# Kernel optimization log

Hardware: AMD Instinct MI355X
Metric: run time of the kernel (lower is better)

Reference implementation:

```python
import jax, jax.numpy as jnp
import numpy as np

Z_DIM = 256
N_MOD = 8
CAT = Z_DIM * N_MOD          # 2048
YS = 1024
B = 4096
EPS = 1e-5


def _layer_norm(x, g, b):
    mu = jnp.mean(x, axis=-1, keepdims=True)
    var = jnp.mean((x - mu) ** 2, axis=-1, keepdims=True)
    return (x - mu) * jax.lax.rsqrt(var + EPS) * g + b


def setup_inputs() -> dict:
    key = jax.random.key(0)
    ks = jax.random.split(key, 16)
    s_cat = 1.0 / np.sqrt(CAT)
    s_ys = 1.0 / np.sqrt(YS)
    return {
        "z_stack": jax.random.normal(ks[0], (N_MOD, B, Z_DIM), jnp.float32),
        "Wq": jax.random.normal(ks[1], (CAT, CAT), jnp.float32) * s_cat,
        "bq": jnp.zeros((CAT,), jnp.float32),
        "Wk": jax.random.normal(ks[2], (CAT, CAT), jnp.float32) * s_cat,
        "bk": jnp.zeros((CAT,), jnp.float32),
        "Wv": jax.random.normal(ks[3], (CAT, CAT), jnp.float32) * s_cat,
        "bv": jnp.zeros((CAT,), jnp.float32),
        "W1": jax.random.normal(ks[4], (CAT, YS), jnp.float32) * s_cat,
        "b1": jnp.zeros((YS,), jnp.float32),
        "W2": jax.random.normal(ks[5], (YS, CAT), jnp.float32) * s_ys,
        "b2": jnp.zeros((CAT,), jnp.float32),
        "ln1_g": jnp.ones((CAT,), jnp.float32),
        "ln1_b": jnp.zeros((CAT,), jnp.float32),
        "ln2_g": jnp.ones((CAT,), jnp.float32),
        "ln2_b": jnp.zeros((CAT,), jnp.float32),
        "Wys": jax.random.normal(ks[6], (CAT, YS), jnp.float32) * s_cat,
        "bys": jnp.zeros((YS,), jnp.float32),
        "Ws": jax.random.normal(ks[7], (N_MOD, YS, Z_DIM), jnp.float32) * s_ys,
        "bs": jnp.zeros((N_MOD, Z_DIM), jnp.float32),
    }


def reference(z_stack, Wq, bq, Wk, bk, Wv, bv, W1, b1, W2, b2,
              ln1_g, ln1_b, ln2_g, ln2_b, Wys, bys, Ws, bs):
    M, Bn, Zd = z_stack.shape
    # torch.cat(z, dim=1): [B, M*Zd]
    x = jnp.transpose(z_stack, (1, 0, 2)).reshape(Bn, M * Zd)
    # self-attention over the batch dim (unscaled, as in source)
    q = x @ Wq + bq
    k = x @ Wk + bk
    v = x @ Wv + bv
    attended = jax.nn.softmax(q @ k.T, axis=-1) @ v  # [B, B] scores
    # dropout is identity in eval mode
    x = _layer_norm(x + attended, ln1_g, ln1_b)
    h = jax.nn.gelu(x @ W1 + b1, approximate=False) @ W2 + b2
    h = _layer_norm(x + h, ln2_g, ln2_b)
    yb = h @ Wys + bys                               # [B, YS]
    # per-module scaling layers, stacked output [M, B, Zd]
    y = jnp.einsum('bs,msz->mbz', yb, Ws) + bs[:, None, :]
    return y
```

## Files before the change

kernel.cpp:

```cpp
#include <hip/hip_runtime.h>
#include <hip/hip_bf16.h>
#include <cstdint>
#include <cstddef>
#include <math.h>

typedef __bf16 bf16x8 __attribute__((ext_vector_type(8)));
typedef float  f32x4  __attribute__((ext_vector_type(4)));

#define DEVI __device__ __forceinline__

static constexpr int BB = 4096;
static constexpr int CD = 2048;
static constexpr int ZD = 256;

DEVI unsigned short f2bf(float f) {
  __bf16 h = (__bf16)f;
  return __builtin_bit_cast(unsigned short, h);
}
DEVI float bf2f(unsigned short u) {
  return (float)__builtin_bit_cast(__bf16, u);
}

DEVI void gload_lds16(const void* g, void* l) {
  __builtin_amdgcn_global_load_lds(
      (__attribute__((address_space(1))) void*)(g),
      (__attribute__((address_space(3))) void*)(l), 16, 0, 0);
}

__global__ __launch_bounds__(256) void pack_x(
    const float* __restrict__ z, float* __restrict__ x,
    unsigned short* __restrict__ xh, unsigned short* __restrict__ xl) {
  const int i = (blockIdx.x * 256 + threadIdx.x) * 4;
  const int m  = i >> 20;
  const int r  = i & 1048575;
  const int b  = r >> 8;
  const int zd = r & 255;
  const float4 v = *(const float4*)(z + i);
  const size_t o = (size_t)b * CD + m * ZD + zd;
  *(float4*)(x + o) = v;
  ushort4 h, l;
  h.x = f2bf(v.x); l.x = f2bf(v.x - bf2f(h.x));
  h.y = f2bf(v.y); l.y = f2bf(v.y - bf2f(h.y));
  h.z = f2bf(v.z); l.z = f2bf(v.z - bf2f(h.z));
  h.w = f2bf(v.w); l.w = f2bf(v.w - bf2f(h.w));
  *(ushort4*)(xh + o) = h;
  *(ushort4*)(xl + o) = l;
}

template<bool LO>
__global__ void transpose_split(const float* __restrict__ in,
                                unsigned short* __restrict__ oh,
                                unsigned short* __restrict__ ol,
                                int R, int C) {
  __shared__ float tile[32][33];
  const int c0 = blockIdx.x * 32, r0 = blockIdx.y * 32;
  const int tx = threadIdx.x, ty = threadIdx.y;
#pragma unroll
  for (int k = 0; k < 4; ++k)
    tile[ty + 8 * k][tx] = in[(size_t)(r0 + ty + 8 * k) * C + (c0 + tx)];
  __syncthreads();
#pragma unroll
  for (int k = 0; k < 4; ++k) {
    const float f = tile[tx][ty + 8 * k];
    const size_t o = (size_t)(c0 + ty + 8 * k) * R + (r0 + tx);
    const unsigned short h = f2bf(f);
    oh[o] = h;
    if constexpr (LO) ol[o] = f2bf(f - bf2f(h));
  }
}

__global__ void transpose_bf16(const unsigned short* __restrict__ in,
                               unsigned short* __restrict__ outp, int R, int C) {
  __shared__ unsigned short tile[32][33];
  const int c0 = blockIdx.x * 32, r0 = blockIdx.y * 32;
  const int tx = threadIdx.x, ty = threadIdx.y;
#pragma unroll
  for (int k = 0; k < 4; ++k)
    tile[ty + 8 * k][tx] = in[(size_t)(r0 + ty + 8 * k) * C + (c0 + tx)];
  __syncthreads();
#pragma unroll
  for (int k = 0; k < 4; ++k)
    outp[(size_t)(c0 + ty + 8 * k) * R + (r0 + tx)] = tile[tx][ty + 8 * k];
}

template<int EP, bool SPLIT>
__global__ __launch_bounds__(256) void gemm_bt(
    const unsigned short* __restrict__ Ah, const unsigned short* __restrict__ Al,
    const unsigned short* __restrict__ Bh, const unsigned short* __restrict__ Bl,
    const float* __restrict__ bias,
    float* __restrict__ Cf, unsigned short* __restrict__ Cb,
    unsigned short* __restrict__ Cb2,
    int M, int N, int K) {
  constexpr int NT = SPLIT ? 4 : 2;
  __shared__ unsigned short lds[NT][128 * 32];
  const int t = threadIdx.x;
  const int lane = t & 63;
  const int w = t >> 6;
  const int wr = (w >> 1) * 64, wc = (w & 1) * 64;
  const int lr = lane & 15, kg = lane >> 4;
  const size_t Ar0 = (size_t)blockIdx.y * 128;
  const size_t Br0 = (size_t)blockIdx.x * 128;

  f32x4 acc[4][4] = {};

  for (int k0 = 0; k0 < K; k0 += 32) {
#pragma unroll
    for (int rnd = 0; rnd < 2; ++rnd) {
      const int e = t * 8 + rnd * 2048;
      const int row = e >> 5, col = e & 31;
      const size_t ga = (Ar0 + row) * (size_t)K + (k0 + col);
      const size_t gb = (Br0 + row) * (size_t)K + (k0 + col);
      const int lo = (w << 9) + rnd * 2048;
      gload_lds16(Ah + ga, &lds[0][lo]);
      gload_lds16(Bh + gb, &lds[1][lo]);
      if constexpr (SPLIT) {
        gload_lds16(Al + ga, &lds[2][lo]);
        gload_lds16(Bl + gb, &lds[3][lo]);
      }
    }
    __syncthreads();
    bf16x8 ah[4], bh[4], al[4], bl[4];
#pragma unroll
    for (int i = 0; i < 4; ++i) {
      ah[i] = *(const bf16x8*)&lds[0][((wr + i * 16 + lr) << 5) + (kg << 3)];
      bh[i] = *(const bf16x8*)&lds[1][((wc + i * 16 + lr) << 5) + (kg << 3)];
      if constexpr (SPLIT) {
        al[i] = *(const bf16x8*)&lds[2][((wr + i * 16 + lr) << 5) + (kg << 3)];
        bl[i] = *(const bf16x8*)&lds[3][((wc + i * 16 + lr) << 5) + (kg << 3)];
      }
    }
#pragma unroll
    for (int i = 0; i < 4; ++i)
#pragma unroll
      for (int j = 0; j < 4; ++j) {
        acc[i][j] = __builtin_amdgcn_mfma_f32_16x16x32_bf16(ah[i], bh[j], acc[i][j], 0, 0, 0);
        if constexpr (SPLIT) {
          acc[i][j] = __builtin_amdgcn_mfma_f32_16x16x32_bf16(ah[i], bl[j], acc[i][j], 0, 0, 0);
          acc[i][j] = __builtin_amdgcn_mfma_f32_16x16x32_bf16(al[i], bh[j], acc[i][j], 0, 0, 0);
        }
      }
    __syncthreads();
  }

  const int rb = (int)Ar0 + wr + (lane >> 4) * 4;
  const int cb = (int)Br0 + wc + lr;
#pragma unroll
  for (int i = 0; i < 4; ++i) {
#pragma unroll
    for (int j = 0; j < 4; ++j) {
      const int col = cb + j * 16;
      const float bsv = bias ? bias[col] : 0.0f;
#pragma unroll
      for (int q = 0; q < 4; ++q) {
        const int row = rb + i * 16 + q;
        const float val = acc[i][j][q] + bsv;
        const size_t o = (size_t)row * N + col;
        if constexpr (EP == 0) {
          Cf[o] = val;
        } else if constexpr (EP == 1) {
          Cb[o] = f2bf(val);
        } else if constexpr (EP == 2) {
          const float ge = 0.5f * val * (1.0f + erff(val * 0.70710678118654752f));
          Cb[o] = f2bf(ge);
        } else if constexpr (EP == 3) {
          const unsigned short h = f2bf(val);
          Cb[o] = h;
          Cb2[o] = f2bf(val - bf2f(h));
        } else {
          const size_t oo = (size_t)(col >> 8) * ((size_t)BB * ZD)
                          + (size_t)row * ZD + (col & 255);
          Cf[oo] = val;
        }
      }
    }
  }
}

__global__ __launch_bounds__(256) void softmax_rows(const float* __restrict__ S,
                                                    unsigned short* __restrict__ P) {
  const int row = blockIdx.x;
  const int t = threadIdx.x;
  const int lane = t & 63, w = t >> 6;
  const float* s = S + (size_t)row * 4096;
  float4 v[4];
  float mx = -3.4e38f;
#pragma unroll
  for (int i = 0; i < 4; ++i) {
    v[i] = *(const float4*)(s + (size_t)(t + 256 * i) * 4);
    mx = fmaxf(mx, fmaxf(fmaxf(v[i].x, v[i].y), fmaxf(v[i].z, v[i].w)));
  }
#pragma unroll
  for (int off = 32; off >= 1; off >>= 1) mx = fmaxf(mx, __shfl_xor(mx, off));
  __shared__ float redm[4], redsum[4];
  if (lane == 0) redm[w] = mx;
  __syncthreads();
  mx = fmaxf(fmaxf(redm[0], redm[1]), fmaxf(redm[2], redm[3]));
  float sum = 0.f;
#pragma unroll
  for (int i = 0; i < 4; ++i) {
    v[i].x = expf(v[i].x - mx);
    v[i].y = expf(v[i].y - mx);
    v[i].z = expf(v[i].z - mx);
    v[i].w = expf(v[i].w - mx);
    sum += v[i].x + v[i].y + v[i].z + v[i].w;
  }
#pragma unroll
  for (int off = 32; off >= 1; off >>= 1) sum += __shfl_xor(sum, off);
  if (lane == 0) redsum[w] = sum;
  __syncthreads();
  sum = redsum[0] + redsum[1] + redsum[2] + redsum[3];
  const float inv = 1.0f / sum;
  unsigned short* p = P + (size_t)row * 4096;
#pragma unroll
  for (int i = 0; i < 4; ++i) {
    ushort4 u;
    u.x = f2bf(v[i].x * inv);
    u.y = f2bf(v[i].y * inv);
    u.z = f2bf(v[i].z * inv);
    u.w = f2bf(v[i].w * inv);
    *(ushort4*)(p + (size_t)(t + 256 * i) * 4) = u;
  }
}

template<bool WF32>
__global__ __launch_bounds__(256) void ln_fused(
    const float* __restrict__ a, const float* __restrict__ b,
    const float* __restrict__ g, const float* __restrict__ be,
    float* __restrict__ of, unsigned short* __restrict__ ob) {
  const int row = blockIdx.x;
  const int t = threadIdx.x;
  const int lane = t & 63, w = t >> 6;
  const float* ar = a + (size_t)row * 2048;
  const float* br = b + (size_t)row * 2048;
  float4 x[2];
  float s = 0.f, ss = 0.f;
#pragma unroll
  for (int i = 0; i < 2; ++i) {
    const int o = (t + 256 * i) * 4;
    const float4 av = *(const float4*)(ar + o);
    const float4 bv = *(const float4*)(br + o);
    x[i].x = av.x + bv.x; x[i].y = av.y + bv.y;
    x[i].z = av.z + bv.z; x[i].w = av.w + bv.w;
    s  += x[i].x + x[i].y + x[i].z + x[i].w;
    ss += x[i].x * x[i].x + x[i].y * x[i].y + x[i].z * x[i].z + x[i].w * x[i].w;
  }
#pragma unroll
  for (int off = 32; off >= 1; off >>= 1) {
    s  += __shfl_xor(s, off);
    ss += __shfl_xor(ss, off);
  }
  __shared__ float rs[4], rss[4];
  if (lane == 0) { rs[w] = s; rss[w] = ss; }
  __syncthreads();
  s  = rs[0] + rs[1] + rs[2] + rs[3];
  ss = rss[0] + rss[1] + rss[2] + rss[3];
  const float mu  = s * (1.0f / 2048.0f);
  const float var = ss * (1.0f / 2048.0f) - mu * mu;
  const float inv = rsqrtf(var + 1e-5f);
#pragma unroll
  for (int i = 0; i < 2; ++i) {
    const int o = (t + 256 * i) * 4;
    const float4 gv  = *(const float4*)(g + o);
    const float4 bev = *(const float4*)(be + o);
    float4 y;
    y.x = (x[i].x - mu) * inv * gv.x + bev.x;
    y.y = (x[i].y - mu) * inv * gv.y + bev.y;
    y.z = (x[i].z - mu) * inv * gv.z + bev.z;
    y.w = (x[i].w - mu) * inv * gv.w + bev.w;
    if constexpr (WF32) *(float4*)(of + (size_t)row * 2048 + o) = y;
    ushort4 u;
    u.x = f2bf(y.x); u.y = f2bf(y.y); u.z = f2bf(y.z); u.w = f2bf(y.w);
    *(ushort4*)(ob + (size_t)row * 2048 + o) = u;
  }
}

extern "C" void kernel_launch(void* const* d_in, const int* in_sizes, int n_in,
                              void* d_out, int out_size, void* d_ws, size_t ws_size,
                              hipStream_t stream) {
  (void)in_sizes; (void)n_in; (void)out_size;
  const float* z    = (const float*)d_in[0];
  const float* Wq   = (const float*)d_in[1];
  const float* bq   = (const float*)d_in[2];
  const float* Wk   = (const float*)d_in[3];
  const float* bk   = (const float*)d_in[4];
  const float* Wv   = (const float*)d_in[5];
  const float* bv   = (const float*)d_in[6];
  const float* W1   = (const float*)d_in[7];
  const float* b1   = (const float*)d_in[8];
  const float* W2   = (const float*)d_in[9];
  const float* b2   = (const float*)d_in[10];
  const float* ln1g = (const float*)d_in[11];
  const float* ln1b = (const float*)d_in[12];
  const float* ln2g = (const float*)d_in[13];
  const float* ln2b = (const float*)d_in[14];
  const float* Wys  = (const float*)d_in[15];
  const float* bys  = (const float*)d_in[16];
  const float* Ws   = (const float*)d_in[17];
  const float* bs   = (const float*)d_in[18];
  float* out = (float*)d_out;
  char* ws = (char*)d_ws;

  const size_t off_x    = 0;
  const size_t off_x2bf = 0;
  const size_t off_ybbf = 16777216;
  const size_t R2       = 33554432;
  const size_t off_xhi  = R2;
  const size_t off_xlo  = R2 + 16777216;
  const size_t off_wqh  = R2 + 33554432;
  const size_t off_wql  = off_wqh + 8388608;
  const size_t off_wkh  = off_wql + 8388608;
  const size_t off_wkl  = off_wkh + 8388608;
  const size_t off_wv   = off_wkl + 8388608;
  const size_t off_S    = R2;
  const size_t off_x1f  = R2;
  const size_t off_x1bf = R2 + 33554432;
  const size_t R3       = 109051904;
  const size_t off_w1t  = R3;
  const size_t off_w2t  = R3 + 4194304;
  const size_t off_wyst = R3 + 8388608;
  const size_t off_wst  = R3 + 12582912;
  const size_t R4       = 125829120;
  const size_t off_qh   = R4;
  const size_t off_ql   = R4 + 16777216;
  const size_t off_kh   = R4 + 33554432;
  const size_t off_kl   = R4 + 50331648;
  const size_t off_P    = R4;
  const size_t off_att  = R4 + 33554432;
  const size_t off_h2   = R4;
  const size_t R5       = 192937984;
  const size_t off_vbf  = R5;
  const size_t off_vt   = R5 + 16777216;
  const size_t off_hmid = R5;
  if (ws_size < 226492416u) return;

#define F32P(o) ((float*)(ws + (o)))
#define BFP(o)  ((unsigned short*)(ws + (o)))

  const dim3 tb(32, 8);

  pack_x<<<8192, 256, 0, stream>>>(z, F32P(off_x), BFP(off_xhi), BFP(off_xlo));
  transpose_split<true ><<<dim3(64, 64), tb, 0, stream>>>(Wq, BFP(off_wqh), BFP(off_wql), 2048, 2048);
  transpose_split<true ><<<dim3(64, 64), tb, 0, stream>>>(Wk, BFP(off_wkh), BFP(off_wkl), 2048, 2048);
  transpose_split<false><<<dim3(64, 64), tb, 0, stream>>>(Wv, BFP(off_wv), nullptr, 2048, 2048);
  transpose_split<false><<<dim3(32, 64), tb, 0, stream>>>(W1, BFP(off_w1t), nullptr, 2048, 1024);
  transpose_split<false><<<dim3(64, 32), tb, 0, stream>>>(W2, BFP(off_w2t), nullptr, 1024, 2048);
  transpose_split<false><<<dim3(32, 64), tb, 0, stream>>>(Wys, BFP(off_wyst), nullptr, 2048, 1024);
  for (int m = 0; m < 8; ++m)
    transpose_split<false><<<dim3(8, 32), tb, 0, stream>>>(
        Ws + (size_t)m * 262144, BFP(off_wst) + (size_t)m * 262144, nullptr, 1024, 256);

  gemm_bt<3, true ><<<dim3(16, 32), 256, 0, stream>>>(BFP(off_xhi), BFP(off_xlo),
      BFP(off_wqh), BFP(off_wql), bq, nullptr, BFP(off_qh), BFP(off_ql), 4096, 2048, 2048);
  gemm_bt<3, true ><<<dim3(16, 32), 256, 0, stream>>>(BFP(off_xhi), BFP(off_xlo),
      BFP(off_wkh), BFP(off_wkl), bk, nullptr, BFP(off_kh), BFP(off_kl), 4096, 2048, 2048);
  gemm_bt<1, false><<<dim3(16, 32), 256, 0, stream>>>(BFP(off_xhi), nullptr,
      BFP(off_wv), nullptr, bv, nullptr, BFP(off_vbf), nullptr, 4096, 2048, 2048);
  transpose_bf16<<<dim3(64, 128), tb, 0, stream>>>(BFP(off_vbf), BFP(off_vt), 4096, 2048);

  gemm_bt<0, true ><<<dim3(32, 32), 256, 0, stream>>>(BFP(off_qh), BFP(off_ql),
      BFP(off_kh), BFP(off_kl), nullptr, F32P(off_S), nullptr, nullptr, 4096, 4096, 2048);
  softmax_rows<<<4096, 256, 0, stream>>>(F32P(off_S), BFP(off_P));
  gemm_bt<0, false><<<dim3(16, 32), 256, 0, stream>>>(BFP(off_P), nullptr,
      BFP(off_vt), nullptr, nullptr, F32P(off_att), nullptr, nullptr, 4096, 2048, 4096);
  ln_fused<true ><<<4096, 256, 0, stream>>>(F32P(off_x), F32P(off_att), ln1g, ln1b,
      F32P(off_x1f), BFP(off_x1bf));

  gemm_bt<2, false><<<dim3(8, 32), 256, 0, stream>>>(BFP(off_x1bf), nullptr,
      BFP(off_w1t), nullptr, b1, nullptr, BFP(off_hmid), nullptr, 4096, 1024, 2048);
  gemm_bt<0, false><<<dim3(16, 32), 256, 0, stream>>>(BFP(off_hmid), nullptr,
      BFP(off_w2t), nullptr, b2, F32P(off_h2), nullptr, nullptr, 4096, 2048, 1024);
  ln_fused<false><<<4096, 256, 0, stream>>>(F32P(off_x1f), F32P(off_h2), ln2g, ln2b,
      nullptr, BFP(off_x2bf));

  gemm_bt<1, false><<<dim3(8, 32), 256, 0, stream>>>(BFP(off_x2bf), nullptr,
      BFP(off_wyst), nullptr, bys, nullptr, BFP(off_ybbf), nullptr, 4096, 1024, 2048);
  gemm_bt<4, false><<<dim3(16, 32), 256, 0, stream>>>(BFP(off_ybbf), nullptr,
      BFP(off_wst), nullptr, bs, out, nullptr, nullptr, 4096, 2048, 1024);
}
```

Before: 887.9 us.

## Fuse Q/K projections into one split-bf16 GEMM with 256x256 pipelined kernel

Packs hi/lo bf16 halves of x and of the Q/K weights side by side along K, so the three-term split-precision product becomes one plain bf16 GEMM over an extended K. A new 256x256-tile, 512-thread kernel with double-buffered direct-to-LDS loads, XOR swizzle, phased barriers and setprio computes Q and K together, then the QK^T scores. The goal is to drop the separate SPLIT GEMM launches, raise MFMA utilisation and cut repeated operand loads. In exchange it needs 128KB of dynamic LDS, uses a hard-coded K schedule and grid remap, and the workspace layout is reorganised.

```diff
diff --git a/kernel.cpp b/kernel.cpp
--- a/kernel.cpp
+++ b/kernel.cpp
@@ -29,29 +29,29 @@
 
 __global__ __launch_bounds__(256) void pack_x(
     const float* __restrict__ z, float* __restrict__ x,
-    unsigned short* __restrict__ xh, unsigned short* __restrict__ xl) {
+    unsigned short* __restrict__ x2) {
   const int i = (blockIdx.x * 256 + threadIdx.x) * 4;
   const int m  = i >> 20;
   const int r  = i & 1048575;
   const int b  = r >> 8;
   const int zd = r & 255;
   const float4 v = *(const float4*)(z + i);
-  const size_t o = (size_t)b * CD + m * ZD + zd;
-  *(float4*)(x + o) = v;
+  const size_t o32 = (size_t)b * CD + m * ZD + zd;
+  *(float4*)(x + o32) = v;
   ushort4 h, l;
   h.x = f2bf(v.x); l.x = f2bf(v.x - bf2f(h.x));
   h.y = f2bf(v.y); l.y = f2bf(v.y - bf2f(h.y));
   h.z = f2bf(v.z); l.z = f2bf(v.z - bf2f(h.z));
   h.w = f2bf(v.w); l.w = f2bf(v.w - bf2f(h.w));
-  *(ushort4*)(xh + o) = h;
-  *(ushort4*)(xl + o) = l;
+  const size_t o2 = (size_t)b * 4096 + m * ZD + zd;
+  *(ushort4*)(x2 + o2) = h;
+  *(ushort4*)(x2 + o2 + 2048) = l;
 }
 
 template<bool LO>
 __global__ void transpose_split(const float* __restrict__ in,
                                 unsigned short* __restrict__ oh,
-                                unsigned short* __restrict__ ol,
-                                int R, int C) {
+                                int R, int C, int ldo) {
   __shared__ float tile[32][33];
   const int c0 = blockIdx.x * 32, r0 = blockIdx.y * 32;
   const int tx = threadIdx.x, ty = threadIdx.y;
@@ -62,10 +62,10 @@
 #pragma unroll
   for (int k = 0; k < 4; ++k) {
     const float f = tile[tx][ty + 8 * k];
-    const size_t o = (size_t)(c0 + ty + 8 * k) * R + (r0 + tx);
+    const size_t o = (size_t)(c0 + ty + 8 * k) * ldo + (r0 + tx);
     const unsigned short h = f2bf(f);
     oh[o] = h;
-    if constexpr (LO) ol[o] = f2bf(f - bf2f(h));
+    if constexpr (LO) oh[o + R] = f2bf(f - bf2f(h));
   }
 }
 
@@ -83,16 +83,196 @@
     outp[(size_t)(c0 + ty + 8 * k) * R + (r0 + tx)] = tile[tx][ty + 8 * k];
 }
 
-template<int EP, bool SPLIT>
+#define DOMFMA(QI, QJ, AF, BF)                                            \
+  {                                                                       \
+    _Pragma("unroll") for (int ks = 0; ks < 2; ++ks) {                    \
+      _Pragma("unroll") for (int f = 0; f < 4; ++f) {                     \
+        _Pragma("unroll") for (int g = 0; g < 2; ++g) {                   \
+          acc[(QI) * 4 + f][(QJ) * 2 + g] =                               \
+              __builtin_amdgcn_mfma_f32_16x16x32_bf16(                    \
+                  AF[f][ks], BF[g][ks], acc[(QI) * 4 + f][(QJ) * 2 + g],  \
+                  0, 0, 0);                                               \
+        }                                                                 \
+      }                                                                   \
+    }                                                                     \
+  }
+
+#define PH_SYNC()                                         \
+  do {                                                    \
+    __builtin_amdgcn_s_barrier();                         \
+    asm volatile("s_waitcnt lgkmcnt(0)" ::: "memory");    \
+    __builtin_amdgcn_sched_barrier(0);                    \
+    __builtin_amdgcn_s_setprio(1);                        \
+  } while (0)
+
+#define PH_END()                                          \
+  do {                                                    \
+    __builtin_amdgcn_s_setprio(0);                        \
+    __builtin_amdgcn_sched_barrier(0);                    \
+    __builtin_amdgcn_s_barrier();                         \
+  } while (0)
+
+template<int EP>
+__global__ __launch_bounds__(512, 2) void gemm256(
+    const unsigned short* __restrict__ A,
+    const unsigned short* __restrict__ Bt,
+    const float* __restrict__ bq, const float* __restrict__ bk,
+    float* __restrict__ Cf,
+    unsigned short* __restrict__ Oa, unsigned short* __restrict__ Ob) {
+  extern __shared__ char lds[];
+  constexpr int NK = 96;
+  const int t = threadIdx.x;
+  const int lane = t & 63;
+  const int w = t >> 6;
+  const int wm = w >> 2, wn = w & 3;
+  const int lr = lane & 15, kg = lane >> 4;
+  const int bid = (blockIdx.x & 7) * 32 + (blockIdx.x >> 3);
+  const int bx = bid & 15, by = bid >> 4;
+  const int Ar0 = by * 256, Br0 = bx * 256;
+
+  auto stage = [&](const unsigned short* __restrict__ src, int row0, int kk,
+                   int dst_off) {
+    const int L = t << 4;
+    const int Lp = L ^ (((L >> 9) & 1) << 5);
+    const int row = Lp >> 7, colb = Lp & 127;
+    const char* g = (const char*)src + ((size_t)(row0 + row) * 4096 + kk) * 2 + colb;
+    gload_lds16(g, lds + dst_off + ((t >> 6) << 10));
+  };
+  auto rdA = [&](const char* buf, int qi, int f, int ks) {
+    int L = ((qi * 64 + f * 16 + lr) << 7) + ks * 64 + kg * 16;
+    L ^= ((L >> 9) & 1) << 5;
+    return *(const bf16x8*)(buf + wm * 16384 + L);
+  };
+  auto rdB = [&](const char* buf, int qj, int g, int ks) {
+    int L = ((wn * 64 + qj * 32 + g * 16 + lr) << 7) + ks * 64 + kg * 16;
+    L ^= ((L >> 9) & 1) << 5;
+    return *(const bf16x8*)(buf + 32768 + L);
+  };
+  auto kA = [](int k0) { return k0 - ((k0 >> 11) == 2 ? 4096 : 0); };
+  auto kB = [](int k0) { return k0 - ((k0 >> 11) >= 1 ? 2048 : 0); };
+
+  f32x4 acc[8][4] = {};
+  bf16x8 af[4][2], b0[2][2], b1[2][2];
+
+  {
+    stage(A,  Ar0 + 0,   kA(0), 0);
+    stage(A,  Ar0 + 64,  kA(0), 8192);
+    stage(A,  Ar0 + 128, kA(0), 16384);
+    stage(A,  Ar0 + 192, kA(0), 24576);
+    stage(Bt, Br0 + 0,   kB(0), 32768);
+    stage(Bt, Br0 + 64,  kB(0), 40960);
+    stage(Bt, Br0 + 128, kB(0), 49152);
+    stage(Bt, Br0 + 192, kB(0), 57344);
+    stage(A,  Ar0 + 0,   kA(64), 65536 + 0);
+    stage(A,  Ar0 + 128, kA(64), 65536 + 16384);
+    stage(Bt, Br0 + 0,   kB(64), 65536 + 32768);
+    stage(Bt, Br0 + 64,  kB(64), 65536 + 40960);
+    stage(Bt, Br0 + 128, kB(64), 65536 + 49152);
+    stage(Bt, Br0 + 192, kB(64), 65536 + 57344);
+    asm volatile("s_waitcnt vmcnt(6)" ::: "memory");
+    __builtin_amdgcn_sched_barrier(0);
+    __builtin_amdgcn_s_barrier();
+  }
+
+  for (int tt = 0; tt < NK; ++tt) {
+    const int cur = tt & 1;
+    const char* buf = lds + cur * 65536;
+    const int curo = cur * 65536, nxto = (cur ^ 1) * 65536;
+    const int k1 = (tt + 1) * 64, k2 = (tt + 2) * 64;
+
+#pragma unroll
+    for (int f = 0; f < 4; ++f)
+#pragma unroll
+      for (int ks = 0; ks < 2; ++ks) af[f][ks] = rdA(buf, 0, f, ks);
+#pragma unroll
+    for (int g = 0; g < 2; ++g)
+#pragma unroll
+      for (int ks = 0; ks < 2; ++ks) b0[g][ks] = rdB(buf, 0, g, ks);
+    if (tt + 1 < NK) {
+      stage(A, Ar0 + 64,  kA(k1), nxto + 8192);
+      stage(A, Ar0 + 192, kA(k1), nxto + 24576);
+    }
+    PH_SYNC();
+    DOMFMA(0, 0, af, b0);
+    PH_END();
+
+#pragma unroll
+    for (int g = 0; g < 2; ++g)
+#pragma unroll
+      for (int ks = 0; ks < 2; ++ks) b1[g][ks] = rdB(buf, 1, g, ks);
+    if (tt + 2 < NK) {
+      stage(A, Ar0 + 0,   kA(k2), curo + 0);
+      stage(A, Ar0 + 128, kA(k2), curo + 16384);
+    }
+    PH_SYNC();
+    DOMFMA(0, 1, af, b1);
+    PH_END();
+
+#pragma unroll
+    for (int f = 0; f < 4; ++f)
+#pragma unroll
+      for (int ks = 0; ks < 2; ++ks) af[f][ks] = rdA(buf, 1, f, ks);
+    if (tt + 2 < NK) {
+      stage(Bt, Br0 + 0,  kB(k2), curo + 32768);
+      stage(Bt, Br0 + 64, kB(k2), curo + 40960);
+    }
+    PH_SYNC();
+    DOMFMA(1, 0, af, b0);
+    PH_END();
+
+    if (tt + 2 < NK) {
+      stage(Bt, Br0 + 128, kB(k2), curo + 49152);
+      stage(Bt, Br0 + 192, kB(k2), curo + 57344);
+      asm volatile("s_waitcnt vmcnt(6)" ::: "memory");
+    } else {
+      asm volatile("s_waitcnt vmcnt(0)" ::: "memory");
+    }
+    __builtin_amdgcn_sched_barrier(0);
+    PH_SYNC();
+    DOMFMA(1, 1, af, b1);
+    PH_END();
+  }
+
+  const int rbase = Ar0 + wm * 128 + kg * 4;
+  const int cbase = Br0 + wn * 64 + lr;
+#pragma unroll
+  for (int rf = 0; rf < 8; ++rf) {
+#pragma unroll
+    for (int cf = 0; cf < 4; ++cf) {
+      const int col = cbase + cf * 16;
+#pragma unroll
+      for (int q = 0; q < 4; ++q) {
+        const int row = rbase + rf * 16 + q;
+        float val = acc[rf][cf][q];
+        if constexpr (EP == 0) {
+          Cf[(size_t)row * 4096 + col] = val;
+        } else {
+          if (col < 2048) {
+            val += bq[col];
+            const unsigned short h = f2bf(val);
+            Oa[(size_t)row * 4096 + col] = h;
+            Oa[(size_t)row * 4096 + 2048 + col] = f2bf(val - bf2f(h));
+          } else {
+            const int c2 = col - 2048;
+            val += bk[c2];
+            const unsigned short h = f2bf(val);
+            Ob[(size_t)row * 4096 + c2] = h;
+            Ob[(size_t)row * 4096 + 2048 + c2] = f2bf(val - bf2f(h));
+          }
+        }
+      }
+    }
+  }
+}
+
+template<int EP>
 __global__ __launch_bounds__(256) void gemm_bt(
-    const unsigned short* __restrict__ Ah, const unsigned short* __restrict__ Al,
-    const unsigned short* __restrict__ Bh, const unsigned short* __restrict__ Bl,
+    const unsigned short* __restrict__ Ah,
+    const unsigned short* __restrict__ Bh,
     const float* __restrict__ bias,
     float* __restrict__ Cf, unsigned short* __restrict__ Cb,
-    unsigned short* __restrict__ Cb2,
-    int M, int N, int K) {
-  constexpr int NT = SPLIT ? 4 : 2;
-  __shared__ unsigned short lds[NT][128 * 32];
+    int M, int N, int K, int lda, int ldb) {
+  __shared__ unsigned short lds[2][128 * 32];
   const int t = threadIdx.x;
   const int lane = t & 63;
   const int w = t >> 6;
@@ -108,37 +288,24 @@
     for (int rnd = 0; rnd < 2; ++rnd) {
       const int e = t * 8 + rnd * 2048;
       const int row = e >> 5, col = e & 31;
-      const size_t ga = (Ar0 + row) * (size_t)K + (k0 + col);
-      const size_t gb = (Br0 + row) * (size_t)K + (k0 + col);
+      const size_t ga = (Ar0 + row) * (size_t)lda + (k0 + col);
+      const size_t gb = (Br0 + row) * (size_t)ldb + (k0 + col);
       const int lo = (w << 9) + rnd * 2048;
       gload_lds16(Ah + ga, &lds[0][lo]);
       gload_lds16(Bh + gb, &lds[1][lo]);
-      if constexpr (SPLIT) {
-        gload_lds16(Al + ga, &lds[2][lo]);
-        gload_lds16(Bl + gb, &lds[3][lo]);
-      }
     }
     __syncthreads();
-    bf16x8 ah[4], bh[4], al[4], bl[4];
+    bf16x8 ah[4], bh[4];
 #pragma unroll
     for (int i = 0; i < 4; ++i) {
       ah[i] = *(const bf16x8*)&lds[0][((wr + i * 16 + lr) << 5) + (kg << 3)];
       bh[i] = *(const bf16x8*)&lds[1][((wc + i * 16 + lr) << 5) + (kg << 3)];
-      if constexpr (SPLIT) {
-        al[i] = *(const bf16x8*)&lds[2][((wr + i * 16 + lr) << 5) + (kg << 3)];
-        bl[i] = *(const bf16x8*)&lds[3][((wc + i * 16 + lr) << 5) + (kg << 3)];
-      }
     }
 #pragma unroll
     for (int i = 0; i < 4; ++i)
 #pragma unroll
-      for (int j = 0; j < 4; ++j) {
+      for (int j = 0; j < 4; ++j)
         acc[i][j] = __builtin_amdgcn_mfma_f32_16x16x32_bf16(ah[i], bh[j], acc[i][j], 0, 0, 0);
-        if constexpr (SPLIT) {
-          acc[i][j] = __builtin_amdgcn_mfma_f32_16x16x32_bf16(ah[i], bl[j], acc[i][j], 0, 0, 0);
-          acc[i][j] = __builtin_amdgcn_mfma_f32_16x16x32_bf16(al[i], bh[j], acc[i][j], 0, 0, 0);
-        }
-      }
     __syncthreads();
   }
 
@@ -162,10 +329,6 @@
         } else if constexpr (EP == 2) {
           const float ge = 0.5f * val * (1.0f + erff(val * 0.70710678118654752f));
           Cb[o] = f2bf(ge);
-        } else if constexpr (EP == 3) {
-          const unsigned short h = f2bf(val);
-          Cb[o] = h;
-          Cb2[o] = f2bf(val - bf2f(h));
         } else {
           const size_t oo = (size_t)(col >> 8) * ((size_t)BB * ZD)
                           + (size_t)row * ZD + (col & 255);
@@ -300,80 +463,71 @@
   float* out = (float*)d_out;
   char* ws = (char*)d_ws;
 
+  const size_t MB = 1048576;
   const size_t off_x    = 0;
-  const size_t off_x2bf = 0;
-  const size_t off_ybbf = 16777216;
-  const size_t R2       = 33554432;
-  const size_t off_xhi  = R2;
-  const size_t off_xlo  = R2 + 16777216;
-  const size_t off_wqh  = R2 + 33554432;
-  const size_t off_wql  = off_wqh + 8388608;
-  const size_t off_wkh  = off_wql + 8388608;
-  const size_t off_wkl  = off_wkh + 8388608;
-  const size_t off_wv   = off_wkl + 8388608;
-  const size_t off_S    = R2;
-  const size_t off_x1f  = R2;
-  const size_t off_x1bf = R2 + 33554432;
-  const size_t R3       = 109051904;
-  const size_t off_w1t  = R3;
-  const size_t off_w2t  = R3 + 4194304;
-  const size_t off_wyst = R3 + 8388608;
-  const size_t off_wst  = R3 + 12582912;
-  const size_t R4       = 125829120;
-  const size_t off_qh   = R4;
-  const size_t off_ql   = R4 + 16777216;
-  const size_t off_kh   = R4 + 33554432;
-  const size_t off_kl   = R4 + 50331648;
-  const size_t off_P    = R4;
-  const size_t off_att  = R4 + 33554432;
-  const size_t off_h2   = R4;
-  const size_t R5       = 192937984;
-  const size_t off_vbf  = R5;
-  const size_t off_vt   = R5 + 16777216;
-  const size_t off_hmid = R5;
-  if (ws_size < 226492416u) return;
+  const size_t off_h2   = 0;
+  const size_t off_x2   = 32 * MB;
+  const size_t off_Bqk  = 64 * MB;
+  const size_t off_S    = 32 * MB;
+  const size_t off_Aq   = 96 * MB;
+  const size_t off_P    = 96 * MB;
+  const size_t off_x1f  = 96 * MB;
+  const size_t off_Btk  = 128 * MB;
+  const size_t off_att  = 128 * MB;
+  const size_t off_hmid = 128 * MB;
+  const size_t off_ybbf = 136 * MB;
+  const size_t off_Vbf  = 160 * MB;
+  const size_t off_x1bf = 160 * MB;
+  const size_t off_Vt   = 176 * MB;
+  const size_t off_x2bf = 176 * MB;
+  const size_t off_Wvt  = 192 * MB;
+  const size_t off_W1t  = 200 * MB;
+  const size_t off_W2t  = 204 * MB;
+  const size_t off_Wyst = 208 * MB;
+  const size_t off_Wst  = 212 * MB;
+  if (ws_size < 216 * MB) return;
 
 #define F32P(o) ((float*)(ws + (o)))
 #define BFP(o)  ((unsigned short*)(ws + (o)))
 
   const dim3 tb(32, 8);
 
-  pack_x<<<8192, 256, 0, stream>>>(z, F32P(off_x), BFP(off_xhi), BFP(off_xlo));
-  transpose_split<true ><<<dim3(64, 64), tb, 0, stream>>>(Wq, BFP(off_wqh), BFP(off_wql), 2048, 2048);
-  transpose_split<true ><<<dim3(64, 64), tb, 0, stream>>>(Wk, BFP(off_wkh), BFP(off_wkl), 2048, 2048);
-  transpose_split<false><<<dim3(64, 64), tb, 0, stream>>>(Wv, BFP(off_wv), nullptr, 2048, 2048);
-  transpose_split<false><<<dim3(32, 64), tb, 0, stream>>>(W1, BFP(off_w1t), nullptr, 2048, 1024);
-  transpose_split<false><<<dim3(64, 32), tb, 0, stream>>>(W2, BFP(off_w2t), nullptr, 1024, 2048);
-  transpose_split<false><<<dim3(32, 64), tb, 0, stream>>>(Wys, BFP(off_wyst), nullptr, 2048, 1024);
+  pack_x<<<8192, 256, 0, stream>>>(z, F32P(off_x), BFP(off_x2));
+  transpose_split<true ><<<dim3(64, 64), tb, 0, stream>>>(Wq, BFP(off_Bqk), 2048, 2048, 4096);
+  transpose_split<true ><<<dim3(64, 64), tb, 0, stream>>>(Wk, BFP(off_Bqk) + (size_t)2048 * 4096, 2048, 2048, 4096);
+  transpose_split<false><<<dim3(64, 64), tb, 0, stream>>>(Wv, BFP(off_Wvt), 2048, 2048, 2048);
+  transpose_split<false><<<dim3(32, 64), tb, 0, stream>>>(W1, BFP(off_W1t), 2048, 1024, 2048);
+  transpose_split<false><<<dim3(64, 32), tb, 0, stream>>>(W2, BFP(off_W2t), 1024, 2048, 1024);
+  transpose_split<false><<<dim3(32, 64), tb, 0, stream>>>(Wys, BFP(off_Wyst), 2048, 1024, 2048);
   for (int m = 0; m < 8; ++m)
     transpose_split<false><<<dim3(8, 32), tb, 0, stream>>>(
-        Ws + (size_t)m * 262144, BFP(off_wst) + (size_t)m * 262144, nullptr, 1024, 256);
-
-  gemm_bt<3, true ><<<dim3(16, 32), 256, 0, stream>>>(BFP(off_xhi), BFP(off_xlo),
-      BFP(off_wqh), BFP(off_wql), bq, nullptr, BFP(off_qh), BFP(off_ql), 4096, 2048, 2048);
-  gemm_bt<3, true ><<<dim3(16, 32), 256, 0, stream>>>(BFP(off_xhi), BFP(off_xlo),
-      BFP(off_wkh), BFP(off_wkl), bk, nullptr, BFP(off_kh), BFP(off_kl), 4096, 2048, 2048);
-  gemm_bt<1, false><<<dim3(16, 32), 256, 0, stream>>>(BFP(off_xhi), nullptr,
-      BFP(off_wv), nullptr, bv, nullptr, BFP(off_vbf), nullptr, 4096, 2048, 2048);
-  transpose_bf16<<<dim3(64, 128), tb, 0, stream>>>(BFP(off_vbf), BFP(off_vt), 4096, 2048);
-
-  gemm_bt<0, true ><<<dim3(32, 32), 256, 0, stream>>>(BFP(off_qh), BFP(off_ql),
-      BFP(off_kh), BFP(off_kl), nullptr, F32P(off_S), nullptr, nullptr, 4096, 4096, 2048);
+        Ws + (size_t)m * 262144, BFP(off_Wst) + (size_t)m * 262144, 1024, 256, 1024);
+
+  gemm_bt<1><<<dim3(16, 32), 256, 0, stream>>>(BFP(off_x2), BFP(off_Wvt), bv,
+      nullptr, BFP(off_Vbf), 4096, 2048, 2048, 4096, 2048);
+  transpose_bf16<<<dim3(64, 128), tb, 0, stream>>>(BFP(off_Vbf), BFP(off_Vt), 4096, 2048);
+
+  gemm256<1><<<256, 512, 131072, stream>>>(BFP(off_x2), BFP(off_Bqk), bq, bk,
+      nullptr, BFP(off_Aq), BFP(off_Btk));
+
+  gemm256<0><<<256, 512, 131072, stream>>>(BFP(off_Aq), BFP(off_Btk), nullptr, nullptr,
+      F32P(off_S), nullptr, nullptr);
+
   softmax_rows<<<4096, 256, 0, stream>>>(F32P(off_S), BFP(off_P));
-  gemm_bt<0, false><<<dim3(16, 32), 256, 0, stream>>>(BFP(off_P), nullptr,
-      BFP(off_vt), nullptr, nullptr, F32P(off_att), nullptr, nullptr, 4096, 2048, 4096);
+  gemm_bt<0><<<dim3(16, 32), 256, 0, stream>>>(BFP(off_P), BFP(off_Vt), nullptr,
+      F32P(off_att), nullptr, 4096, 2048, 4096, 4096, 4096);
   ln_fused<true ><<<4096, 256, 0, stream>>>(F32P(off_x), F32P(off_att), ln1g, ln1b,
       F32P(off_x1f), BFP(off_x1bf));
 
-  gemm_bt<2, false><<<dim3(8, 32), 256, 0, stream>>>(BFP(off_x1bf), nullptr,
-      BFP(off_w1t), nullptr, b1, nullptr, BFP(off_hmid), nullptr, 4096, 1024, 2048);
-  gemm_bt<0, false><<<dim3(16, 32), 256, 0, stream>>>(BFP(off_hmid), nullptr,
-      BFP(off_w2t), nullptr, b2, F32P(off_h2), nullptr, nullptr, 4096, 2048, 1024);
+  gemm_bt<2><<<dim3(8, 32), 256, 0, stream>>>(BFP(off_x1bf), BFP(off_W1t), b1,
+      nullptr, BFP(off_hmid), 4096, 1024, 2048, 2048, 2048);
+  gemm_bt<0><<<dim3(16, 32), 256, 0, stream>>>(BFP(off_hmid), BFP(off_W2t), b2,
+      F32P(off_h2), nullptr, 4096, 2048, 1024, 1024, 1024);
   ln_fused<false><<<4096, 256, 0, stream>>>(F32P(off_x1f), F32P(off_h2), ln2g, ln2b,
       nullptr, BFP(off_x2bf));
 
-  gemm_bt<1, false><<<dim3(8, 32), 256, 0, stream>>>(BFP(off_x2bf), nullptr,
-      BFP(off_wyst), nullptr, bys, nullptr, BFP(off_ybbf), nullptr, 4096, 1024, 2048);
-  gemm_bt<4, false><<<dim3(16, 32), 256, 0, stream>>>(BFP(off_ybbf), nullptr,
-      BFP(off_wst), nullptr, bs, out, nullptr, nullptr, 4096, 2048, 1024);
-}
+  gemm_bt<1><<<dim3(8, 32), 256, 0, stream>>>(BFP(off_x2bf), BFP(off_Wyst), bys,
+      nullptr, BFP(off_ybbf), 4096, 1024, 2048, 2048, 2048);
+  gemm_bt<4><<<dim3(16, 32), 256, 0, stream>>>(BFP(off_ybbf), BFP(off_Wst), bs,
+      out, nullptr, 4096, 2048, 1024, 1024, 1024);
+}
```

Result: faster. 832.5 us (-6.2%).
